# Kernel tuning notes

Hardware: AMD Instinct MI355X
Metric: run time of the kernel (lower is better)

Reference implementation:

```python
import jax, jax.numpy as jnp
import numpy as np

B, T_CHAR, E, N_CHARS, T_TAG = 128, 256, 512, 128, 32


def _rn(k, shape, scale=1.0):
    return jax.random.normal(k, shape, dtype=jnp.float32) * scale


def setup_inputs() -> dict:
    key = jax.random.key(0)
    ks = jax.random.split(key, 24)
    W = 0.05  # param init scale
    tgt_idx = jax.random.randint(ks[4], (B, T_CHAR), 0, N_CHARS)
    return {
        "char_encoding": _rn(ks[0], (B, T_CHAR, E)),
        "char_hn": _rn(ks[1], (2, B, E // 2)),
        "char_cn": _rn(ks[2], (2, B, E // 2)),
        "tag_encoding": _rn(ks[3], (B, T_TAG, E)),
        "true_output_seq": jax.nn.one_hot(tgt_idx, N_CHARS, dtype=jnp.float32),
        # LSTMCell(n_chars -> E), torch gate order i,f,g,o
        "lstm_Wih": _rn(ks[5], (4 * E, N_CHARS), W),
        "lstm_Whh": _rn(ks[6], (4 * E, E), W),
        "lstm_bih": jnp.zeros((4 * E,), jnp.float32),
        "lstm_bhh": jnp.zeros((4 * E,), jnp.float32),
        # char MultiheadAttention (1 head)
        "ca_Wq": _rn(ks[7], (E, E), W), "ca_Wk": _rn(ks[8], (E, E), W), "ca_Wv": _rn(ks[9], (E, E), W),
        "ca_bq": jnp.zeros((E,), jnp.float32), "ca_bk": jnp.zeros((E,), jnp.float32), "ca_bv": jnp.zeros((E,), jnp.float32),
        "ca_Wo": _rn(ks[10], (E, E), W), "ca_bo": jnp.zeros((E,), jnp.float32),
        # tag MultiheadAttention (1 head)
        "ta_Wq": _rn(ks[11], (E, E), W), "ta_Wk": _rn(ks[12], (E, E), W), "ta_Wv": _rn(ks[13], (E, E), W),
        "ta_bq": jnp.zeros((E,), jnp.float32), "ta_bk": jnp.zeros((E,), jnp.float32), "ta_bv": jnp.zeros((E,), jnp.float32),
        "ta_Wo": _rn(ks[14], (E, E), W), "ta_bo": jnp.zeros((E,), jnp.float32),
        # output Linear(2E -> n_chars)
        "out_W": _rn(ks[15], (N_CHARS, 2 * E), W),
        "out_b": jnp.zeros((N_CHARS,), jnp.float32),
    }


def _attend(h, enc_K, enc_V, Wq, bq, Wo, bo):
    # single-head torch MHA: scale query by 1/sqrt(embed_dim)
    q = (h @ Wq.T + bq) * (1.0 / np.sqrt(E))          # [B,E]
    scores = jnp.einsum('be,bse->bs', q, enc_K)        # [B,S]
    a = jax.nn.softmax(scores, axis=-1)
    ctx = jnp.einsum('bs,bse->be', a, enc_V)           # [B,E]
    return ctx @ Wo.T + bo


def reference(char_encoding, char_hn, char_cn, tag_encoding, true_output_seq,
              lstm_Wih, lstm_Whh, lstm_bih, lstm_bhh,
              ca_Wq, ca_Wk, ca_Wv, ca_bq, ca_bk, ca_bv, ca_Wo, ca_bo,
              ta_Wq, ta_Wk, ta_Wv, ta_bq, ta_bk, ta_bv, ta_Wo, ta_bo,
              out_W, out_b):
    # K/V projections are step-invariant: hoist out of the decode loop
    Kc = char_encoding @ ca_Wk.T + ca_bk               # [B,Tc,E]
    Vc = char_encoding @ ca_Wv.T + ca_bv
    Kt = tag_encoding @ ta_Wk.T + ta_bk                # [B,Tt,E]
    Vt = tag_encoding @ ta_Wv.T + ta_bv

    h0 = jnp.concatenate([char_hn[0], char_hn[1]], axis=-1)  # [B,E]
    c0 = jnp.concatenate([char_cn[0], char_cn[1]], axis=-1)

    # teacher forcing: step 0 input is zeros, step t uses true_output_seq[:, t, :]
    x0 = jnp.zeros((char_encoding.shape[0], true_output_seq.shape[-1]), char_encoding.dtype)
    xs = jnp.concatenate([x0[:, None, :], true_output_seq[:, 1:, :]], axis=1)
    xs = jnp.swapaxes(xs, 0, 1)                        # [T,B,n_chars]

    def step(carry, x_t):
        h, c = carry
        gates = x_t @ lstm_Wih.T + lstm_bih + h @ lstm_Whh.T + lstm_bhh
        i, f, g, o = jnp.split(gates, 4, axis=-1)
        c1 = jax.nn.sigmoid(f) * c + jax.nn.sigmoid(i) * jnp.tanh(g)
        h1 = jax.nn.sigmoid(o) * jnp.tanh(c1)
        char_ctx = _attend(h1, Kc, Vc, ca_Wq, ca_bq, ca_Wo, ca_bo)
        tag_ctx = _attend(h1, Kt, Vt, ta_Wq, ta_bq, ta_Wo, ta_bo)
        agg = jax.nn.relu(jnp.concatenate([char_ctx, tag_ctx], axis=-1))  # [B,2E]
        out = agg @ out_W.T + out_b                    # [B,n_chars]
        return (h1, c1), out

    _, outs = jax.lax.scan(step, (h0, c0), xs)         # outs: [T,B,n_chars]
    return jnp.swapaxes(outs, 0, 1)                    # [B,T,n_chars]
```

## Files before the change

kernel.cpp:

```cpp
#include <hip/hip_runtime.h>
#include <cstdint>

#define BB 128
#define TT 256
#define EE 512
#define NC 128
#define STAG 32

#define NWG 64
#define SB 4
#define SC 16
#define NKV 2304

using bf = unsigned short;
typedef __attribute__((ext_vector_type(8))) short short8;
typedef __attribute__((ext_vector_type(8))) unsigned short ushort8;
typedef __attribute__((ext_vector_type(16))) float f32x16;
typedef unsigned long long u64;

static __device__ __forceinline__ float bfu(bf x) { return __uint_as_float(((uint32_t)x) << 16); }
static __device__ __forceinline__ uint32_t f2bf(float f) {
    uint32_t u = __float_as_uint(f);
    return (u + 0x7FFFu + ((u >> 16) & 1u)) >> 16;
}
static __device__ __forceinline__ float sigmoidf_(float x) { return 1.f / (1.f + expf(-x)); }

static __device__ __forceinline__ uint4 pack8bf(float4 a, float4 b) {
    uint4 o;
    o.x = (f2bf(a.y) << 16) | f2bf(a.x);
    o.y = (f2bf(a.w) << 16) | f2bf(a.z);
    o.z = (f2bf(b.y) << 16) | f2bf(b.x);
    o.w = (f2bf(b.w) << 16) | f2bf(b.z);
    return o;
}

static __device__ __forceinline__ uint32_t relu2bf(uint32_t x) {
    uint32_t lo = x & 0xFFFFu, hi = x >> 16;
    lo = (lo & 0x8000u) ? 0u : lo;
    hi = (hi & 0x8000u) ? 0u : hi;
    return lo | (hi << 16);
}

__global__ void diag_ws(float* __restrict__ out, float v, int n) {
    int i = blockIdx.x * 256 + threadIdx.x;
    if (i < n) out[i] = v;
}

__global__ void conv_f2b(const float* __restrict__ s, bf* __restrict__ d, int n) {
    int i = (blockIdx.x * 256 + threadIdx.x) * 4;
    if (i >= n) return;
    float4 v = *(const float4*)(s + i);
    ushort4 o = { (bf)f2bf(v.x), (bf)f2bf(v.y), (bf)f2bf(v.z), (bf)f2bf(v.w) };
    *(ushort4*)(d + i) = o;
}

struct W8 { const float* p[8]; };
__global__ void conv_w8(W8 ws, bf* __restrict__ d) {
    int m = blockIdx.y;
    int i = (blockIdx.x * 256 + threadIdx.x) * 4;
    float4 v = *(const float4*)(ws.p[m] + i);
    ushort4 o = { (bf)f2bf(v.x), (bf)f2bf(v.y), (bf)f2bf(v.z), (bf)f2bf(v.w) };
    *(ushort4*)(d + (size_t)m * 262144 + i) = o;
}

__global__ void h0_pack(const float* __restrict__ hn, bf* __restrict__ Hext) {
    int id = blockIdx.x * 256 + threadIdx.x;
    int b = id >> 9, e = id & 511;
    float v = (e < 256) ? hn[(size_t)b * 256 + e] : hn[(size_t)(BB + b) * 256 + (e - 256)];
    Hext[((size_t)(e >> 3) * BB + b) * 8 + (e & 7)] = (bf)f2bf(v);
}

__global__ void bt_prep2(const float* __restrict__ Whh, bf* __restrict__ Btg2) {
    int id = blockIdx.x * 256 + threadIdx.x;
    int row = id >> 6, chunk = (id & 63) * 8;
    int cg = row >> 7, n = row & 127;
    int r = (n & 3) * 512 + cg * 32 + (n >> 2);
    const float* src = Whh + (size_t)r * 512 + chunk;
    ushort8 o;
#pragma unroll
    for (int i = 0; i < 8; ++i) o[i] = (bf)f2bf(src[i]);
    *(ushort8*)(Btg2 + (size_t)row * 512 + chunk) = o;
}

__global__ void x_prep(const float* __restrict__ tos, int* __restrict__ xidx,
                       float* __restrict__ xval) {
    int id = blockIdx.x * 256 + threadIdx.x;
    int t = id >> 7, b = id & 127;
    int idx = 0; float val = 0.f;
    if (t > 0) {
        const float* row = tos + ((size_t)b * TT + t) * NC;
        for (int k = 0; k < NC; ++k) {
            float v = row[k];
            if (v != 0.f) { idx = k; val = v; }
        }
    }
    xidx[(size_t)t * BB + b] = idx;
    xval[(size_t)t * BB + b] = val;
}

static __device__ __forceinline__ int lds_off(int row, int colbyte) {
    return row * 128 + (colbyte ^ ((row & 7) << 4));
}

template <int MODE>
static __device__ __forceinline__ void worker_gemm(
    const float* __restrict__ Af, const bf* __restrict__ Wb,
    const float* __restrict__ bias, bf* __restrict__ C,
    int bm, int bn, char* smem)
{
    bf* As = (bf*)smem;
    bf* Bs = (bf*)(smem + 16384);
    const int tid = threadIdx.x;
    const int w = tid >> 6, l = tid & 63;
    const int wr = (w >> 1) * 64, wc = (w & 1) * 64;

    f32x16 acc[2][2];
#pragma unroll
    for (int i = 0; i < 2; ++i)
#pragma unroll
        for (int j = 0; j < 2; ++j)
#pragma unroll
            for (int r = 0; r < 16; ++r) acc[i][j][r] = 0.f;

    const int srow = tid >> 3;
    const int scolb = (tid & 7) * 16;
    const int scole = (tid & 7) * 8;

    for (int k0 = 0; k0 < 512; k0 += 64) {
#pragma unroll
        for (int pass = 0; pass < 4; ++pass) {
            int row = pass * 32 + srow;
            const float* ap = Af + (size_t)(bm + row) * 512 + k0 + scole;
            float4 v0 = *(const float4*)ap;
            float4 v1 = *(const float4*)(ap + 4);
            *(uint4*)((char*)As + lds_off(row, scolb)) = pack8bf(v0, v1);
            uint4 vb = *(const uint4*)(Wb + (size_t)(bn + row) * 512 + k0 + scole);
            *(uint4*)((char*)Bs + lds_off(row, scolb)) = vb;
        }
        __syncthreads();
#pragma unroll
        for (int kt = 0; kt < 4; ++kt) {
            const int cb = kt * 32 + (l >> 5) * 16;
            short8 af[2], bfr[2];
#pragma unroll
            for (int i = 0; i < 2; ++i) {
                af[i]  = *(const short8*)((char*)As + lds_off(wr + i * 32 + (l & 31), cb));
                bfr[i] = *(const short8*)((char*)Bs + lds_off(wc + i * 32 + (l & 31), cb));
            }
#pragma unroll
            for (int i = 0; i < 2; ++i)
#pragma unroll
                for (int j = 0; j < 2; ++j)
                    acc[i][j] = __builtin_amdgcn_mfma_f32_32x32x16_bf16(af[i], bfr[j], acc[i][j], 0, 0, 0);
        }
        __syncthreads();
    }

#pragma unroll
    for (int i = 0; i < 2; ++i)
#pragma unroll
        for (int j = 0; j < 2; ++j) {
            int n = bn + wc + j * 32 + (l & 31);
            float bv = bias[n];
#pragma unroll
            for (int r = 0; r < 16; ++r) {
                int m = bm + wr + i * 32 + (r & 3) + 8 * (r >> 2) + 4 * (l >> 5);
                bf v = (bf)f2bf(acc[i][j][r] + bv);
                if constexpr (MODE == 0) {
                    C[(size_t)m * 512 + n] = v;
                } else if constexpr (MODE == 1) {
                    int b = m >> 8, s = m & 255;
                    C[((size_t)b * 512 + n) * 256 + s] = v;
                } else {
                    int b = m >> 5, s = m & 31;
                    C[((size_t)b * 512 + n) * 32 + s] = v;
                }
            }
        }
}

struct KVArgs {
    const float *Ac, *At;
    const bf *WcK, *WcV, *WtK, *WtV;
    const float *bcK, *bcV, *btK, *btV;
    bf *Kc, *VcT, *Kt, *VtT;
};

__global__ __launch_bounds__(256, 1) void lstm_fused(
    bf* __restrict__ Hext,
    const bf* __restrict__ Btg2,
    const float* __restrict__ Wih,
    const float* __restrict__ bih, const float* __restrict__ bhh,
    const float* __restrict__ cn,
    const int* __restrict__ xidx, const float* __restrict__ xval,
    char* __restrict__ flags,
    KVArgs kv)
{
    __shared__ __align__(16) char smem[66048];

    const int gb = blockIdx.x, tid = threadIdx.x;

    if (gb >= NWG) {
        int w = gb - NWG;
        if (w < 1024) {
            worker_gemm<0>(kv.Ac, kv.WcK, kv.bcK, kv.Kc, (w >> 2) * 128, (w & 3) * 128, smem);
        } else if (w < 2048) {
            int t = w - 1024;
            worker_gemm<1>(kv.Ac, kv.WcV, kv.bcV, kv.VcT, (t >> 2) * 128, (t & 3) * 128, smem);
        } else if (w < 2176) {
            int t = w - 2048;
            worker_gemm<0>(kv.At, kv.WtK, kv.btK, kv.Kt, (t >> 2) * 128, (t & 3) * 128, smem);
        } else {
            int t = w - 2176;
            worker_gemm<2>(kv.At, kv.WtV, kv.btV, kv.VtT, (t >> 2) * 128, (t & 3) * 128, smem);
        }
        return;
    }

    bf*    Alds   = (bf*)smem;
    float* gatesf = (float*)smem;
    bf*    wihtp  = (bf*)(smem + 32768);
    float* biass  = (float*)(smem + 65536);

    const int g = gb;
    const int bh = g >> 4, cg = g & 15;

    for (int x = tid; x < 128 * NC; x += 256) {
        int n = x >> 7, k = x & 127;
        int r = (n & 3) * 512 + cg * 32 + (n >> 2);
        wihtp[k * 128 + n] = (bf)f2bf(Wih[(size_t)r * NC + k]);
    }
    if (tid < 128) {
        int r = (tid & 3) * 512 + cg * 32 + (tid >> 2);
        biass[tid] = bih[r] + bhh[r];
    }

    const int b_loc = tid >> 3, u = tid & 7;
    const int b_glob = bh * 32 + b_loc;
    float creg[4];
    {
        int j0 = cg * 32 + u * 4;
        const float* csrc = (cg < 8) ? (cn + (size_t)b_glob * 256 + j0)
                                     : (cn + (size_t)(BB + b_glob) * 256 + (j0 - 256));
#pragma unroll
        for (int i = 0; i < 4; ++i) creg[i] = csrc[i];
    }

    const int wv = tid >> 6, l = tid & 63;

    short8 breg[32];
    {
        const bf* bsrc = Btg2 + ((size_t)(cg * 128 + wv * 32 + (l & 31)) * 512)
                       + (l >> 5) * 8;
#pragma unroll
        for (int kt = 0; kt < 32; ++kt) breg[kt] = *(const short8*)(bsrc + kt * 16);
    }
    __syncthreads();

    const int sb = tid & 31, sg0 = tid >> 5;
    const int dst_lane = sb | ((sg0 & 1) << 5);
    bf* dstbase = Alds + (size_t)(sg0 >> 1) * 512 + dst_lane * 8;

    u64* Hw = (u64*)Hext;
    const size_t SLABB = (size_t)BB * EE * 2;
    const size_t SLAB64 = (size_t)BB * EE / 4;
    const size_t hst_off = (size_t)(cg * 4 + (u >> 1)) * 256 + b_glob * 2 + (u & 1);
    const bf* ards = Alds + l * 8;

    for (int t = 0; t < TT; ++t) {
        const char* At = (const char*)Hext + (size_t)t * SLABB
                       + (size_t)sg0 * 2048 + (size_t)(bh * 32 + sb) * 16;
        uint4 areg[8];
#pragma unroll
        for (int i = 0; i < 8; ++i) {
            asm volatile("global_load_dwordx4 %0, %1, off sc0 sc1"
                         : "=v"(areg[i]) : "v"(At + (size_t)i * 16384));
        }
        float xv = xval[(size_t)t * BB + b_glob];
        int   xi = xidx[(size_t)t * BB + b_glob];
        asm volatile("s_waitcnt vmcnt(0)" ::: "memory");
        __builtin_amdgcn_sched_barrier(0);
#pragma unroll
        for (int i = 0; i < 8; ++i)
            *(uint4*)(dstbase + (size_t)i * 2048) = areg[i];
        __syncthreads();

        f32x16 acc0, acc1;
#pragma unroll
        for (int i = 0; i < 16; ++i) { acc0[i] = 0.f; acc1[i] = 0.f; }
#pragma unroll
        for (int kt = 0; kt < 32; kt += 2) {
            short8 a0 = *(const short8*)(ards + (size_t)kt * 512);
            short8 a1 = *(const short8*)(ards + (size_t)(kt + 1) * 512);
            acc0 = __builtin_amdgcn_mfma_f32_32x32x16_bf16(a0, breg[kt], acc0, 0, 0, 0);
            acc1 = __builtin_amdgcn_mfma_f32_32x32x16_bf16(a1, breg[kt + 1], acc1, 0, 0, 0);
        }
        __syncthreads();
#pragma unroll
        for (int r = 0; r < 16; ++r) {
            int m = (r & 3) + 8 * (r >> 2) + 4 * (l >> 5);
            gatesf[m * 132 + wv * 32 + (l & 31)] = acc0[r] + acc1[r];
        }
        __syncthreads();

        {
            union { ushort4 v; u64 uu; } hout;
#pragma unroll
            for (int i = 0; i < 4; ++i) {
                int nb = (u * 4 + i) * 4;
                float4 ga  = *(const float4*)&gatesf[b_loc * 132 + nb];
                float4 bb4 = *(const float4*)&biass[nb];
                ushort4 xw = *(const ushort4*)&wihtp[xi * 128 + nb];
                float a0 = ga.x + bb4.x + xv * bfu(xw.x);
                float a1 = ga.y + bb4.y + xv * bfu(xw.y);
                float a2 = ga.z + bb4.z + xv * bfu(xw.z);
                float a3 = ga.w + bb4.w + xv * bfu(xw.w);
                float ig = sigmoidf_(a0);
                float fg = sigmoidf_(a1);
                float gg = tanhf(a2);
                float og = sigmoidf_(a3);
                creg[i] = fg * creg[i] + ig * gg;
                float hnew = og * tanhf(creg[i]);
                hout.v[i] = (bf)f2bf(hnew);
            }
            __hip_atomic_store(Hw + (size_t)(t + 1) * SLAB64 + hst_off, hout.uu,
                               __ATOMIC_RELAXED, __HIP_MEMORY_SCOPE_AGENT);
        }

        if (t + 1 < TT) {
            asm volatile("s_waitcnt vmcnt(0)" ::: "memory");
            __syncthreads();
            char* fb = flags + (size_t)(t + 1) * (SB * 2048) + (size_t)bh * 2048;
            if (tid == 0)
                __hip_atomic_store((int*)(fb + (size_t)cg * 128), 1,
                                   __ATOMIC_RELAXED, __HIP_MEMORY_SCOPE_SYSTEM);
            if (tid < 64) {
                const int* fp = (const int*)(fb + (size_t)(tid & 15) * 128);
                while (true) {
                    int v = __hip_atomic_load(fp, __ATOMIC_RELAXED,
                                              __HIP_MEMORY_SCOPE_SYSTEM);
                    if (__all(v != 0)) break;
                    __builtin_amdgcn_s_sleep(1);
                }
            }
            asm volatile("" ::: "memory");
            __syncthreads();
        }
    }
}

template <int S>
__global__ __launch_bounds__(256, 1) void attn_fused(
    const bf* __restrict__ Hext,
    const bf* __restrict__ Wq, const float* __restrict__ bq,
    const bf* __restrict__ Km,
    const bf* __restrict__ VT,
    const bf* __restrict__ Wo, const float* __restrict__ bo,
    bf* __restrict__ occ)
{
    constexpr int SP = S + 8;
    __shared__ __align__(16) bf    Qs[32][520];
    __shared__ __align__(16) float scs[32][SP];
    __shared__ __align__(16) bf    Ps[32][SP];

    const float QSCALE = 0.044194173824159216f;
    const int t0 = blockIdx.x * 32, b = blockIdx.y;
    const int tid = threadIdx.x, wv = tid >> 6, l = tid & 63;
    const int lm = l & 31, lh = l >> 5;

    {
        f32x16 qa[4];
#pragma unroll
        for (int nt = 0; nt < 4; ++nt)
#pragma unroll
            for (int r = 0; r < 16; ++r) qa[nt][r] = 0.f;
#pragma unroll 4
        for (int kt = 0; kt < 32; ++kt) {
            short8 a = *(const short8*)(Hext
                + (((size_t)(t0 + lm + 1) * 64 + kt * 2 + lh) * 1024 + (size_t)b * 8));
#pragma unroll
            for (int nt = 0; nt < 4; ++nt) {
                int n = wv * 128 + nt * 32 + lm;
                short8 w = *(const short8*)(Wq + (size_t)n * 512 + kt * 16 + lh * 8);
                qa[nt] = __builtin_amdgcn_mfma_f32_32x32x16_bf16(a, w, qa[nt], 0, 0, 0);
            }
        }
#pragma unroll
        for (int nt = 0; nt < 4; ++nt) {
            int n = wv * 128 + nt * 32 + lm;
            float bv = bq[n];
#pragma unroll
            for (int r = 0; r < 16; ++r) {
                int m = (r & 3) + 8 * (r >> 2) + 4 * lh;
                Qs[m][n] = (bf)f2bf((qa[nt][r] + bv) * QSCALE);
            }
        }
    }
    __syncthreads();

    {
        constexpr int NJ = (S == 256) ? 2 : 1;
        f32x16 sa[NJ];
#pragma unroll
        for (int j = 0; j < NJ; ++j)
#pragma unroll
            for (int r = 0; r < 16; ++r) sa[j][r] = 0.f;
#pragma unroll 4
        for (int kt = 0; kt < 32; ++kt) {
            short8 a = *(const short8*)&Qs[lm][kt * 16 + lh * 8];
#pragma unroll
            for (int j = 0; j < NJ; ++j) {
                int s = ((S == 256) ? (wv * 64 + j * 32) : 0) + lm;
                short8 k8 = *(const short8*)(Km + ((size_t)b * S + s) * 512 + kt * 16 + lh * 8);
                sa[j] = __builtin_amdgcn_mfma_f32_32x32x16_bf16(a, k8, sa[j], 0, 0, 0);
            }
        }
#pragma unroll
        for (int j = 0; j < NJ; ++j) {
            int s = ((S == 256) ? (wv * 64 + j * 32) : 0) + lm;
#pragma unroll
            for (int r = 0; r < 16; ++r) {
                int m = (r & 3) + 8 * (r >> 2) + 4 * lh;
                scs[m][s] = sa[j][r];
            }
        }
    }
    __syncthreads();

    {
        int r = tid >> 3, lg = tid & 7;
        float mx = -1e30f;
        for (int c = lg; c < S; c += 8) mx = fmaxf(mx, scs[r][c]);
#pragma unroll
        for (int d = 1; d < 8; d <<= 1) mx = fmaxf(mx, __shfl_xor(mx, d));
        float sum = 0.f;
        for (int c = lg; c < S; c += 8) {
            float e = expf(scs[r][c] - mx);
            scs[r][c] = e;
            sum += e;
        }
#pragma unroll
        for (int d = 1; d < 8; d <<= 1) sum += __shfl_xor(sum, d);
        float inv = 1.f / sum;
        for (int c = lg; c < S; c += 8) Ps[r][c] = (bf)f2bf(scs[r][c] * inv);
    }
    __syncthreads();

    {
        f32x16 ca[4];
#pragma unroll
        for (int nt = 0; nt < 4; ++nt)
#pragma unroll
            for (int r = 0; r < 16; ++r) ca[nt][r] = 0.f;
#pragma unroll
        for (int kt = 0; kt < S / 16; ++kt) {
            short8 a = *(const short8*)&Ps[lm][kt * 16 + lh * 8];
#pragma unroll
            for (int nt = 0; nt < 4; ++nt) {
                int n = wv * 128 + nt * 32 + lm;
                short8 v8 = *(const short8*)(VT + ((size_t)b * 512 + n) * S + kt * 16 + lh * 8);
                ca[nt] = __builtin_amdgcn_mfma_f32_32x32x16_bf16(a, v8, ca[nt], 0, 0, 0);
            }
        }
        __syncthreads();
#pragma unroll
        for (int nt = 0; nt < 4; ++nt) {
            int n = wv * 128 + nt * 32 + lm;
#pragma unroll
            for (int r = 0; r < 16; ++r) {
                int m = (r & 3) + 8 * (r >> 2) + 4 * lh;
                Qs[m][n] = (bf)f2bf(ca[nt][r]);
            }
        }
    }
    __syncthreads();

    {
        f32x16 oa[4];
#pragma unroll
        for (int nt = 0; nt < 4; ++nt)
#pragma unroll
            for (int r = 0; r < 16; ++r) oa[nt][r] = 0.f;
#pragma unroll 4
        for (int kt = 0; kt < 32; ++kt) {
            short8 a = *(const short8*)&Qs[lm][kt * 16 + lh * 8];
#pragma unroll
            for (int nt = 0; nt < 4; ++nt) {
                int n = wv * 128 + nt * 32 + lm;
                short8 w = *(const short8*)(Wo + (size_t)n * 512 + kt * 16 + lh * 8);
                oa[nt] = __builtin_amdgcn_mfma_f32_32x32x16_bf16(a, w, oa[nt], 0, 0, 0);
            }
        }
#pragma unroll
        for (int nt = 0; nt < 4; ++nt) {
            int n = wv * 128 + nt * 32 + lm;
            float bv = bo[n];
#pragma unroll
            for (int r = 0; r < 16; ++r) {
                int m = (r & 3) + 8 * (r >> 2) + 4 * lh;
                occ[((size_t)(t0 + m) * BB + b) * 512 + n] = (bf)f2bf(oa[nt][r] + bv);
            }
        }
    }
}

__global__ __launch_bounds__(256) void gemm_out(
    const bf* __restrict__ A1, const bf* __restrict__ A2,
    const bf* __restrict__ Wo,
    const float* __restrict__ bias, float* __restrict__ out)
{
    __shared__ __align__(16) bf As[128 * 64];
    __shared__ __align__(16) bf Bs[128 * 64];
    const int tid = threadIdx.x;
    const int bm = blockIdx.x * 128;
    const int w = tid >> 6, l = tid & 63;
    const int wr = (w >> 1) * 64, wc = (w & 1) * 64;

    f32x16 acc[2][2];
#pragma unroll
    for (int i = 0; i < 2; ++i)
#pragma unroll
        for (int j = 0; j < 2; ++j)
#pragma unroll
            for (int r = 0; r < 16; ++r) acc[i][j][r] = 0.f;

    const int srow = tid >> 3;
    const int scolb = (tid & 7) * 16;
    const int scole = (tid & 7) * 8;

    for (int k0 = 0; k0 < 1024; k0 += 64) {
        const bf* Asrc = (k0 < 512) ? A1 : A2;
        const int kk = k0 & 511;
#pragma unroll
        for (int pass = 0; pass < 4; ++pass) {
            int row = pass * 32 + srow;
            uint4 va = *(const uint4*)(Asrc + (size_t)(bm + row) * 512 + kk + scole);
            va.x = relu2bf(va.x); va.y = relu2bf(va.y);
            va.z = relu2bf(va.z); va.w = relu2bf(va.w);
            *(uint4*)((char*)As + lds_off(row, scolb)) = va;
            uint4 vb = *(const uint4*)(Wo + (size_t)row * 1024 + k0 + scole);
            *(uint4*)((char*)Bs + lds_off(row, scolb)) = vb;
        }
        __syncthreads();
#pragma unroll
        for (int kt = 0; kt < 4; ++kt) {
            const int cb = kt * 32 + (l >> 5) * 16;
            short8 af[2], bfr[2];
#pragma unroll
            for (int i = 0; i < 2; ++i) {
                af[i]  = *(const short8*)((char*)As + lds_off(wr + i * 32 + (l & 31), cb));
                bfr[i] = *(const short8*)((char*)Bs + lds_off(wc + i * 32 + (l & 31), cb));
            }
#pragma unroll
            for (int i = 0; i < 2; ++i)
#pragma unroll
                for (int j = 0; j < 2; ++j)
                    acc[i][j] = __builtin_amdgcn_mfma_f32_32x32x16_bf16(af[i], bfr[j], acc[i][j], 0, 0, 0);
        }
        __syncthreads();
    }

#pragma unroll
    for (int i = 0; i < 2; ++i)
#pragma unroll
        for (int j = 0; j < 2; ++j) {
            int n = wc + j * 32 + (l & 31);
            float bv = bias[n];
#pragma unroll
            for (int r = 0; r < 16; ++r) {
                int m = bm + wr + i * 32 + (r & 3) + 8 * (r >> 2) + 4 * (l >> 5);
                int tt = m >> 7, bb_ = m & 127;
                out[((size_t)bb_ * TT + tt) * NC + n] = acc[i][j][r] + bv;
            }
        }
}

extern "C" void kernel_launch(void* const* d_in, const int* in_sizes, int n_in,
                              void* d_out, int out_size, void* d_ws, size_t ws_size,
                              hipStream_t stream) {
    const float* char_enc = (const float*)d_in[0];
    const float* char_hn  = (const float*)d_in[1];
    const float* char_cn  = (const float*)d_in[2];
    const float* tag_enc  = (const float*)d_in[3];
    const float* tos      = (const float*)d_in[4];
    const float* Wih = (const float*)d_in[5];
    const float* Whh = (const float*)d_in[6];
    const float* bih = (const float*)d_in[7];
    const float* bhh = (const float*)d_in[8];
    const float* caWq = (const float*)d_in[9],  *caWk = (const float*)d_in[10], *caWv = (const float*)d_in[11];
    const float* cabq = (const float*)d_in[12], *cabk = (const float*)d_in[13], *cabv = (const float*)d_in[14];
    const float* caWo = (const float*)d_in[15], *cabo = (const float*)d_in[16];
    const float* taWq = (const float*)d_in[17], *taWk = (const float*)d_in[18], *taWv = (const float*)d_in[19];
    const float* tabq = (const float*)d_in[20], *tabk = (const float*)d_in[21], *tabv = (const float*)d_in[22];
    const float* taWo = (const float*)d_in[23], *tabo = (const float*)d_in[24];
    const float* outW = (const float*)d_in[25], *outb = (const float*)d_in[26];
    float* out = (float*)d_out;

    const size_t SZ  = (size_t)TT * BB * EE;
    const size_t SZT = (size_t)BB * STAG * EE;
    const size_t SLAB = (size_t)BB * EE;
    const size_t HEXT = SZ + SLAB;
    const size_t FLAGB = (size_t)TT * SB * 2048;

    const size_t NEED = FLAGB + HEXT * 2 + 4 * SZ * 2 + 2 * SZT * 2
                      + (size_t)SC * 128 * EE * 2 + (size_t)TT * BB * 8
                      + (8 * 262144 + 131072) * 2;
    if (ws_size < NEED) {
        diag_ws<<<dim3((out_size + 255) / 256), dim3(256), 0, stream>>>(
            out, (float)((double)ws_size / 1048576.0), out_size);
        return;
    }

    char* w = (char*)d_ws;
    char* flags = w;             w += FLAGB;
    bf* Hext = (bf*)w;           w += HEXT * 2;
    bf* Kc = (bf*)w;             w += SZ * 2;
    bf* VcT = (bf*)w;            w += SZ * 2;
    bf* Occ = (bf*)w;            w += SZ * 2;
    bf* Oct = (bf*)w;            w += SZ * 2;
    bf* Kt = (bf*)w;             w += SZT * 2;
    bf* VtT = (bf*)w;            w += SZT * 2;
    bf* Btg2 = (bf*)w;           w += (size_t)SC * 128 * EE * 2;
    int* xidx = (int*)w;         w += (size_t)TT * BB * 4;
    float* xval = (float*)w;     w += (size_t)TT * BB * 4;
    bf* Wbf = (bf*)w;            w += 8 * 262144 * 2;
    bf* WoutB = (bf*)w;          w += 131072 * 2;

    bf* WbcaK = Wbf + 0 * 262144; bf* WbcaV = Wbf + 1 * 262144;
    bf* WbcaQ = Wbf + 2 * 262144; bf* WbcaO = Wbf + 3 * 262144;
    bf* WbtaK = Wbf + 4 * 262144; bf* WbtaV = Wbf + 5 * 262144;
    bf* WbtaQ = Wbf + 6 * 262144; bf* WbtaO = Wbf + 7 * 262144;

    hipMemsetAsync(flags, 0, FLAGB, stream);
    h0_pack<<<dim3(256), dim3(256), 0, stream>>>(char_hn, Hext);
    bt_prep2<<<dim3(512), dim3(256), 0, stream>>>(Whh, Btg2);
    x_prep<<<dim3(128), dim3(256), 0, stream>>>(tos, xidx, xval);
    W8 w8; w8.p[0] = caWk; w8.p[1] = caWv; w8.p[2] = caWq; w8.p[3] = caWo;
    w8.p[4] = taWk; w8.p[5] = taWv; w8.p[6] = taWq; w8.p[7] = taWo;
    conv_w8<<<dim3(256, 8), dim3(256), 0, stream>>>(w8, Wbf);
    conv_f2b<<<dim3(128), dim3(256), 0, stream>>>(outW, WoutB, 131072);

    KVArgs kv;
    kv.Ac = char_enc; kv.At = tag_enc;
    kv.WcK = WbcaK; kv.WcV = WbcaV; kv.WtK = WbtaK; kv.WtV = WbtaV;
    kv.bcK = cabk; kv.bcV = cabv; kv.btK = tabk; kv.btV = tabv;
    kv.Kc = Kc; kv.VcT = VcT; kv.Kt = Kt; kv.VtT = VtT;
    lstm_fused<<<dim3(NWG + NKV), dim3(256), 0, stream>>>(
        Hext, Btg2, Wih, bih, bhh, char_cn, xidx, xval, flags, kv);

    attn_fused<256><<<dim3(TT / 32, BB), dim3(256), 0, stream>>>(
        Hext, WbcaQ, cabq, Kc, VcT, WbcaO, cabo, Occ);
    attn_fused<32><<<dim3(TT / 32, BB), dim3(256), 0, stream>>>(
        Hext, WbtaQ, tabq, Kt, VtT, WbtaO, tabo, Oct);

    gemm_out<<<dim3(256), dim3(256), 0, stream>>>(Occ, Oct, WoutB, outb, out);
}
```

Before: 1.561 ms.

## Replace per-step flag barrier with sentinel-based data polling on hidden state

```diff
diff --git a/kernel.cpp b/kernel.cpp
--- a/kernel.cpp
+++ b/kernel.cpp
@@ -193,7 +193,6 @@
     const float* __restrict__ bih, const float* __restrict__ bhh,
     const float* __restrict__ cn,
     const int* __restrict__ xidx, const float* __restrict__ xval,
-    char* __restrict__ flags,
     KVArgs kv)
 {
     __shared__ __align__(16) char smem[66048];
@@ -268,17 +267,31 @@
     const bf* ards = Alds + l * 8;
 
     for (int t = 0; t < TT; ++t) {
+        float xv = xval[(size_t)t * BB + b_glob];
+        int   xi = xidx[(size_t)t * BB + b_glob];
+
         const char* At = (const char*)Hext + (size_t)t * SLABB
                        + (size_t)sg0 * 2048 + (size_t)(bh * 32 + sb) * 16;
         uint4 areg[8];
-#pragma unroll
-        for (int i = 0; i < 8; ++i) {
-            asm volatile("global_load_dwordx4 %0, %1, off sc0 sc1"
-                         : "=v"(areg[i]) : "v"(At + (size_t)i * 16384));
-        }
-        float xv = xval[(size_t)t * BB + b_glob];
-        int   xi = xidx[(size_t)t * BB + b_glob];
-        asm volatile("s_waitcnt vmcnt(0)" ::: "memory");
+        while (true) {
+#pragma unroll
+            for (int i = 0; i < 8; ++i) {
+                asm volatile("global_load_dwordx4 %0, %1, off sc0 sc1"
+                             : "=v"(areg[i]) : "v"(At + (size_t)i * 16384));
+            }
+            asm volatile("s_waitcnt vmcnt(0)" ::: "memory");
+            uint32_t bad = 0;
+#pragma unroll
+            for (int i = 0; i < 8; ++i) {
+                uint32_t d0 = areg[i].x, d1 = areg[i].y, d2 = areg[i].z, d3 = areg[i].w;
+                bad |= ((d0 & 0xFFFFu) == 0xFFFFu) | ((d0 >> 16) == 0xFFFFu);
+                bad |= ((d1 & 0xFFFFu) == 0xFFFFu) | ((d1 >> 16) == 0xFFFFu);
+                bad |= ((d2 & 0xFFFFu) == 0xFFFFu) | ((d2 >> 16) == 0xFFFFu);
+                bad |= ((d3 & 0xFFFFu) == 0xFFFFu) | ((d3 >> 16) == 0xFFFFu);
+            }
+            if (!bad) break;
+            __builtin_amdgcn_s_sleep(0);
+        }
         __builtin_amdgcn_sched_barrier(0);
 #pragma unroll
         for (int i = 0; i < 8; ++i)
@@ -327,25 +340,7 @@
                                __ATOMIC_RELAXED, __HIP_MEMORY_SCOPE_AGENT);
         }
 
-        if (t + 1 < TT) {
-            asm volatile("s_waitcnt vmcnt(0)" ::: "memory");
-            __syncthreads();
-            char* fb = flags + (size_t)(t + 1) * (SB * 2048) + (size_t)bh * 2048;
-            if (tid == 0)
-                __hip_atomic_store((int*)(fb + (size_t)cg * 128), 1,
-                                   __ATOMIC_RELAXED, __HIP_MEMORY_SCOPE_SYSTEM);
-            if (tid < 64) {
-                const int* fp = (const int*)(fb + (size_t)(tid & 15) * 128);
-                while (true) {
-                    int v = __hip_atomic_load(fp, __ATOMIC_RELAXED,
-                                              __HIP_MEMORY_SCOPE_SYSTEM);
-                    if (__all(v != 0)) break;
-                    __builtin_amdgcn_s_sleep(1);
-                }
-            }
-            asm volatile("" ::: "memory");
-            __syncthreads();
-        }
+        __syncthreads();
     }
 }
 
@@ -600,9 +595,8 @@
     const size_t SZT = (size_t)BB * STAG * EE;
     const size_t SLAB = (size_t)BB * EE;
     const size_t HEXT = SZ + SLAB;
-    const size_t FLAGB = (size_t)TT * SB * 2048;
-
-    const size_t NEED = FLAGB + HEXT * 2 + 4 * SZ * 2 + 2 * SZT * 2
+
+    const size_t NEED = HEXT * 2 + 4 * SZ * 2 + 2 * SZT * 2
                       + (size_t)SC * 128 * EE * 2 + (size_t)TT * BB * 8
                       + (8 * 262144 + 131072) * 2;
     if (ws_size < NEED) {
@@ -612,7 +606,6 @@
     }
 
     char* w = (char*)d_ws;
-    char* flags = w;             w += FLAGB;
     bf* Hext = (bf*)w;           w += HEXT * 2;
     bf* Kc = (bf*)w;             w += SZ * 2;
     bf* VcT = (bf*)w;            w += SZ * 2;
@@ -631,7 +624,7 @@
     bf* WbtaK = Wbf + 4 * 262144; bf* WbtaV = Wbf + 5 * 262144;
     bf* WbtaQ = Wbf + 6 * 262144; bf* WbtaO = Wbf + 7 * 262144;
 
-    hipMemsetAsync(flags, 0, FLAGB, stream);
+    hipMemsetAsync((char*)Hext + SLAB * 2, 0xFF, SZ * 2, stream);
     h0_pack<<<dim3(256), dim3(256), 0, stream>>>(char_hn, Hext);
     bt_prep2<<<dim3(512), dim3(256), 0, stream>>>(Whh, Btg2);
     x_prep<<<dim3(128), dim3(256), 0, stream>>>(tos, xidx, xval);
@@ -646,7 +639,7 @@
     kv.bcK = cabk; kv.bcV = cabv; kv.btK = tabk; kv.btV = tabv;
     kv.Kc = Kc; kv.VcT = VcT; kv.Kt = Kt; kv.VtT = VtT;
     lstm_fused<<<dim3(NWG + NKV), dim3(256), 0, stream>>>(
-        Hext, Btg2, Wih, bih, bhh, char_cn, xidx, xval, flags, kv);
+        Hext, Btg2, Wih, bih, bhh, char_cn, xidx, xval, kv);
 
     attn_fused<256><<<dim3(TT / 32, BB), dim3(256), 0, stream>>>(
         Hext, WbcaQ, cabq, Kc, VcT, WbcaO, cabo, Occ);
```

After: 1.598 ms. +2.4%, slower.

## Merge char and tag attention into one launch with aliased shared memory

Applied to the files above, without the earlier changes.

```diff
diff --git a/kernel.cpp b/kernel.cpp
--- a/kernel.cpp
+++ b/kernel.cpp
@@ -350,22 +350,24 @@
 }
 
 template <int S>
-__global__ __launch_bounds__(256, 1) void attn_fused(
+static __device__ void attn_side(
     const bf* __restrict__ Hext,
     const bf* __restrict__ Wq, const float* __restrict__ bq,
     const bf* __restrict__ Km,
     const bf* __restrict__ VT,
     const bf* __restrict__ Wo, const float* __restrict__ bo,
-    bf* __restrict__ occ)
+    bf* __restrict__ occ,
+    int t0, int b, int tid, char* smem)
 {
-    constexpr int SP = S + 8;
-    __shared__ __align__(16) bf    Qs[32][520];
-    __shared__ __align__(16) float scs[32][SP];
-    __shared__ __align__(16) bf    Ps[32][SP];
+    constexpr int SP = S + 4;
+    constexpr int PP = S + 8;
+    bf*    Qs   = (bf*)smem;
+    float* scs  = (float*)(smem + 33280);
+    bf*    Ps   = (bf*)smem;
+    bf*    occs = (bf*)(smem + 33280);
 
     const float QSCALE = 0.044194173824159216f;
-    const int t0 = blockIdx.x * 32, b = blockIdx.y;
-    const int tid = threadIdx.x, wv = tid >> 6, l = tid & 63;
+    const int wv = tid >> 6, l = tid & 63;
     const int lm = l & 31, lh = l >> 5;
 
     {
@@ -392,7 +394,7 @@
 #pragma unroll
             for (int r = 0; r < 16; ++r) {
                 int m = (r & 3) + 8 * (r >> 2) + 4 * lh;
-                Qs[m][n] = (bf)f2bf((qa[nt][r] + bv) * QSCALE);
+                Qs[m * 520 + n] = (bf)f2bf((qa[nt][r] + bv) * QSCALE);
             }
         }
     }
@@ -407,7 +409,7 @@
             for (int r = 0; r < 16; ++r) sa[j][r] = 0.f;
 #pragma unroll 4
         for (int kt = 0; kt < 32; ++kt) {
-            short8 a = *(const short8*)&Qs[lm][kt * 16 + lh * 8];
+            short8 a = *(const short8*)&Qs[lm * 520 + kt * 16 + lh * 8];
 #pragma unroll
             for (int j = 0; j < NJ; ++j) {
                 int s = ((S == 256) ? (wv * 64 + j * 32) : 0) + lm;
@@ -421,7 +423,7 @@
 #pragma unroll
             for (int r = 0; r < 16; ++r) {
                 int m = (r & 3) + 8 * (r >> 2) + 4 * lh;
-                scs[m][s] = sa[j][r];
+                scs[m * SP + s] = sa[j][r];
             }
         }
     }
@@ -430,19 +432,19 @@
     {
         int r = tid >> 3, lg = tid & 7;
         float mx = -1e30f;
-        for (int c = lg; c < S; c += 8) mx = fmaxf(mx, scs[r][c]);
+        for (int c = lg; c < S; c += 8) mx = fmaxf(mx, scs[r * SP + c]);
 #pragma unroll
         for (int d = 1; d < 8; d <<= 1) mx = fmaxf(mx, __shfl_xor(mx, d));
         float sum = 0.f;
         for (int c = lg; c < S; c += 8) {
-            float e = expf(scs[r][c] - mx);
-            scs[r][c] = e;
+            float e = expf(scs[r * SP + c] - mx);
+            scs[r * SP + c] = e;
             sum += e;
         }
 #pragma unroll
         for (int d = 1; d < 8; d <<= 1) sum += __shfl_xor(sum, d);
         float inv = 1.f / sum;
-        for (int c = lg; c < S; c += 8) Ps[r][c] = (bf)f2bf(scs[r][c] * inv);
+        for (int c = lg; c < S; c += 8) Ps[r * PP + c] = (bf)f2bf(scs[r * SP + c] * inv);
     }
     __syncthreads();
 
@@ -454,7 +456,7 @@
             for (int r = 0; r < 16; ++r) ca[nt][r] = 0.f;
 #pragma unroll
         for (int kt = 0; kt < S / 16; ++kt) {
-            short8 a = *(const short8*)&Ps[lm][kt * 16 + lh * 8];
+            short8 a = *(const short8*)&Ps[lm * PP + kt * 16 + lh * 8];
 #pragma unroll
             for (int nt = 0; nt < 4; ++nt) {
                 int n = wv * 128 + nt * 32 + lm;
@@ -469,7 +471,7 @@
 #pragma unroll
             for (int r = 0; r < 16; ++r) {
                 int m = (r & 3) + 8 * (r >> 2) + 4 * lh;
-                Qs[m][n] = (bf)f2bf(ca[nt][r]);
+                Qs[m * 520 + n] = (bf)f2bf(ca[nt][r]);
             }
         }
     }
@@ -483,7 +485,7 @@
             for (int r = 0; r < 16; ++r) oa[nt][r] = 0.f;
 #pragma unroll 4
         for (int kt = 0; kt < 32; ++kt) {
-            short8 a = *(const short8*)&Qs[lm][kt * 16 + lh * 8];
+            short8 a = *(const short8*)&Qs[lm * 520 + kt * 16 + lh * 8];
 #pragma unroll
             for (int nt = 0; nt < 4; ++nt) {
                 int n = wv * 128 + nt * 32 + lm;
@@ -498,10 +500,36 @@
 #pragma unroll
             for (int r = 0; r < 16; ++r) {
                 int m = (r & 3) + 8 * (r >> 2) + 4 * lh;
-                occ[((size_t)(t0 + m) * BB + b) * 512 + n] = (bf)f2bf(oa[nt][r] + bv);
-            }
-        }
-    }
+                occs[m * 520 + n] = (bf)f2bf(oa[nt][r] + bv);
+            }
+        }
+        __syncthreads();
+        int row = tid >> 3, c0 = (tid & 7) * 64;
+        const bf* src = occs + row * 520 + c0;
+        bf* dst = occ + ((size_t)(t0 + row) * BB + b) * 512 + c0;
+#pragma unroll
+        for (int k = 0; k < 8; ++k)
+            *(uint4*)(dst + k * 8) = *(const uint4*)(src + k * 8);
+    }
+}
+
+struct AttnArgs {
+    const bf* Hext;
+    const bf *WcQ, *WcO, *WtQ, *WtO;
+    const float *bcq, *bco, *btq, *bto;
+    const bf *Kc, *VcT, *Kt, *VtT;
+    bf *Occ, *Oct;
+};
+
+__global__ __launch_bounds__(256, 2) void attn_all(AttnArgs a) {
+    __shared__ __align__(16) char smem[66560];
+    const int t0 = blockIdx.x * 32, b = blockIdx.y, tid = threadIdx.x;
+    if (blockIdx.z == 0)
+        attn_side<256>(a.Hext, a.WcQ, a.bcq, a.Kc, a.VcT, a.WcO, a.bco, a.Occ,
+                       t0, b, tid, smem);
+    else
+        attn_side<32>(a.Hext, a.WtQ, a.btq, a.Kt, a.VtT, a.WtO, a.bto, a.Oct,
+                      t0, b, tid, smem);
 }
 
 __global__ __launch_bounds__(256) void gemm_out(
@@ -648,10 +676,13 @@
     lstm_fused<<<dim3(NWG + NKV), dim3(256), 0, stream>>>(
         Hext, Btg2, Wih, bih, bhh, char_cn, xidx, xval, flags, kv);
 
-    attn_fused<256><<<dim3(TT / 32, BB), dim3(256), 0, stream>>>(
-        Hext, WbcaQ, cabq, Kc, VcT, WbcaO, cabo, Occ);
-    attn_fused<32><<<dim3(TT / 32, BB), dim3(256), 0, stream>>>(
-        Hext, WbtaQ, tabq, Kt, VtT, WbtaO, tabo, Oct);
+    AttnArgs aa;
+    aa.Hext = Hext;
+    aa.WcQ = WbcaQ; aa.WcO = WbcaO; aa.WtQ = WbtaQ; aa.WtO = WbtaO;
+    aa.bcq = cabq; aa.bco = cabo; aa.btq = tabq; aa.bto = tabo;
+    aa.Kc = Kc; aa.VcT = VcT; aa.Kt = Kt; aa.VtT = VtT;
+    aa.Occ = Occ; aa.Oct = Oct;
+    attn_all<<<dim3(TT / 32, BB, 2), dim3(256), 0, stream>>>(aa);
 
     gemm_out<<<dim3(256), dim3(256), 0, stream>>>(Occ, Oct, WoutB, outb, out);
 }
```

Result: faster. 1.527 ms (-2.2%).
